# Optimization experiments

Hardware: AMD Instinct MI355X
Metric: run time of the kernel (lower is better)

The kernel has to match this reference:

```python
import jax, jax.numpy as jnp
import numpy as np

B, T, C = 2, 2048, 2048
H, HD = 16, 128  # num_heads, head_dim; inner_dim = H*HD = C
EPS = 1e-8


def _hadamard(n):
    # Sylvester construction, orthonormal scaling 1/sqrt(n)
    h = np.array([[1.0]], dtype=np.float32)
    while h.shape[0] < n:
        h = np.block([[h, h], [h, -h]])
    return jnp.asarray(h / np.sqrt(n), dtype=jnp.float32)


def _round_ste(x):
    # straight-through rounding (matches int8 training-time quantization semantics)
    return x + jax.lax.stop_gradient(jnp.round(x) - x)


def q8_linear(x, w):
    # dynamic per-token int8 activation quant + per-out-channel int8 weight quant
    s_x = jnp.max(jnp.abs(x), axis=-1, keepdims=True) / 127.0 + EPS   # (B,T,1)
    xq = _round_ste(jnp.clip(x / s_x, -127.0, 127.0))
    s_w = jnp.max(jnp.abs(w), axis=-1, keepdims=True) / 127.0 + EPS   # (O,1)
    wq = _round_ste(jnp.clip(w / s_w, -127.0, 127.0))
    return jnp.einsum('btk,ok->bto', xq, wq) * s_x * s_w[:, 0]


def rmsnorm(x, g, eps=1e-6):
    return x * jax.lax.rsqrt(jnp.mean(x * x, axis=-1, keepdims=True) + eps) * g


def apply_rope(x, cos, sin):
    # x: (B,T,H*HD); cos/sin: (T,HD/2); interleaved rotary per head
    b, t, c = x.shape
    xh = x.reshape(b, t, -1, HD)
    x1, x2 = xh[..., 0::2], xh[..., 1::2]
    co = cos[None, :, None, :]
    si = sin[None, :, None, :]
    o1 = x1 * co - x2 * si
    o2 = x1 * si + x2 * co
    out = jnp.stack([o1, o2], axis=-1).reshape(b, t, -1, HD)
    return out.reshape(b, t, c)


def setup_inputs() -> dict:
    key = jax.random.key(0)
    ks = jax.random.split(key, 8)
    hidden_states = jax.random.normal(ks[0], (B, T, C), jnp.float32)
    attention_mask = jax.random.randint(ks[1], (B,), 1, T + 1).astype(jnp.int32)  # valid lengths
    sc = 1.0 / np.sqrt(C)
    wq = jax.random.normal(ks[2], (H * HD, C), jnp.float32) * sc
    wk = jax.random.normal(ks[3], (H * HD, C), jnp.float32) * sc
    wv = jax.random.normal(ks[4], (H * HD, C), jnp.float32) * sc
    wo = jax.random.normal(ks[5], (C, H * HD), jnp.float32) * (1.0 / np.sqrt(H * HD))
    q_gamma = jnp.ones((H * HD,), jnp.float32)
    k_gamma = jnp.ones((H * HD,), jnp.float32)
    inv_freq = 1.0 / (10000.0 ** (np.arange(0, HD, 2, dtype=np.float32) / HD))
    freqs = np.outer(np.arange(T, dtype=np.float32), inv_freq)  # (T, HD/2)
    cos = jnp.asarray(np.cos(freqs), jnp.float32)
    sin = jnp.asarray(np.sin(freqs), jnp.float32)
    return {"hidden_states": hidden_states, "attention_mask": attention_mask,
            "wq": wq, "wk": wk, "wv": wv, "wo": wo,
            "q_gamma": q_gamma, "k_gamma": k_gamma, "cos": cos, "sin": sin}


def reference(hidden_states, attention_mask, wq, wk, wv, wo, q_gamma, k_gamma, cos, sin):
    b, t, c = hidden_states.shape
    q = rmsnorm(q8_linear(hidden_states, wq), q_gamma)
    k = rmsnorm(q8_linear(hidden_states, wk), k_gamma)
    v = q8_linear(hidden_states, wv)
    q = apply_rope(q, cos, sin)
    k = apply_rope(k, cos, sin)
    # (B,T,H*HD) -> (B,H,T,HD)
    q = q.reshape(b, t, H, HD).transpose(0, 2, 1, 3)
    k = k.reshape(b, t, H, HD).transpose(0, 2, 1, 3)
    v = v.reshape(b, t, H, HD).transpose(0, 2, 1, 3)
    # Hadamard rotation of q/k head dims (orthonormal -> preserves qk dot products)
    Hm = _hadamard(HD)
    qh = q @ Hm
    kh = k @ Hm
    scores = jnp.einsum('bhqd,bhkd->bhqk', qh, kh) * (1.0 / np.sqrt(HD))
    # ragged batch mask: keys beyond per-batch valid length are masked out
    valid = jnp.arange(t)[None, :] < attention_mask[:, None]   # (B,T)
    scores = jnp.where(valid[:, None, None, :], scores, -1e9)
    p = jax.nn.softmax(scores, axis=-1)
    o = jnp.einsum('bhqk,bhkd->bhqd', p, v)
    o = o.transpose(0, 2, 1, 3).reshape(b, t, c)
    return q8_linear(o, wo)
```

## Files before the change

kernel.cpp:

```cpp
#include <hip/hip_runtime.h>
#include <stdint.h>

typedef unsigned short u16;
typedef unsigned int u32;
typedef int v4i __attribute__((ext_vector_type(4)));
typedef float v4f __attribute__((ext_vector_type(4)));
typedef short v8s __attribute__((ext_vector_type(8)));

#define Bn 2
#define Tn 2048
#define Cn 2048
#define Hn 16
#define HDn 128

__device__ __forceinline__ float b2f(u16 u) {
    u32 x = ((u32)u) << 16;
    float f;
    __builtin_memcpy(&f, &x, 4);
    return f;
}
__device__ __forceinline__ u16 f2b(float f) {
    u32 x;
    __builtin_memcpy(&x, &f, 4);
    u32 r = (x + 0x7fffu + ((x >> 16) & 1u)) >> 16;
    return (u16)r;
}

__device__ __forceinline__ void async16(const void* g, void* l) {
    __builtin_amdgcn_global_load_lds(
        (const __attribute__((address_space(1))) u32*)g,
        (__attribute__((address_space(3))) u32*)l, 16, 0, 0);
}

__global__ __launch_bounds__(256) void quant_all(
    const float* __restrict__ w0, const float* __restrict__ w1,
    const float* __restrict__ w2, const float* __restrict__ w3,
    const float* __restrict__ hid, int8_t* __restrict__ Q,
    float* __restrict__ S) {
    int r = blockIdx.x;
    const float* src;
    int ro;
    if (r < 2048) { src = w0; ro = r; }
    else if (r < 4096) { src = w1; ro = r - 2048; }
    else if (r < 6144) { src = w2; ro = r - 4096; }
    else if (r < 8192) { src = w3; ro = r - 6144; }
    else { src = hid; ro = r - 8192; }
    const float* x = src + (size_t)ro * Cn;
    int tid = threadIdx.x;
    float4 v0 = ((const float4*)x)[tid * 2];
    float4 v1 = ((const float4*)x)[tid * 2 + 1];
    float a[8] = {v0.x, v0.y, v0.z, v0.w, v1.x, v1.y, v1.z, v1.w};
    float m = 0.f;
#pragma unroll
    for (int i = 0; i < 8; i++) m = fmaxf(m, fabsf(a[i]));
#pragma unroll
    for (int o = 32; o; o >>= 1) m = fmaxf(m, __shfl_xor(m, o));
    __shared__ float sm[4];
    if ((tid & 63) == 0) sm[tid >> 6] = m;
    __syncthreads();
    m = fmaxf(fmaxf(sm[0], sm[1]), fmaxf(sm[2], sm[3]));
    float s = m * (1.0f / 127.0f) + 1e-8f;
    if (tid == 0) S[r] = s;
    u32 lo = 0, hi = 0;
#pragma unroll
    for (int i = 0; i < 8; i++) {
        float q = rintf(fminf(127.f, fmaxf(-127.f, a[i] / s)));
        int qi = (int)q;
        u32 byte = (u32)(qi & 0xff);
        if (i < 4) lo |= byte << (8 * i);
        else hi |= byte << (8 * (i - 4));
    }
    u32* qp = (u32*)(Q + (size_t)r * Cn);
    qp[tid * 2] = lo;
    qp[tid * 2 + 1] = hi;
}

__global__ __launch_bounds__(256) void quant_rows(const float* __restrict__ X,
                                                  int8_t* __restrict__ Q,
                                                  float* __restrict__ S) {
    int r = blockIdx.x;
    const float* x = X + (size_t)r * Cn;
    int tid = threadIdx.x;
    float4 v0 = ((const float4*)x)[tid * 2];
    float4 v1 = ((const float4*)x)[tid * 2 + 1];
    float a[8] = {v0.x, v0.y, v0.z, v0.w, v1.x, v1.y, v1.z, v1.w};
    float m = 0.f;
#pragma unroll
    for (int i = 0; i < 8; i++) m = fmaxf(m, fabsf(a[i]));
#pragma unroll
    for (int o = 32; o; o >>= 1) m = fmaxf(m, __shfl_xor(m, o));
    __shared__ float sm[4];
    if ((tid & 63) == 0) sm[tid >> 6] = m;
    __syncthreads();
    m = fmaxf(fmaxf(sm[0], sm[1]), fmaxf(sm[2], sm[3]));
    float s = m * (1.0f / 127.0f) + 1e-8f;
    if (tid == 0) S[r] = s;
    u32 lo = 0, hi = 0;
#pragma unroll
    for (int i = 0; i < 8; i++) {
        float q = rintf(fminf(127.f, fmaxf(-127.f, a[i] / s)));
        int qi = (int)q;
        u32 byte = (u32)(qi & 0xff);
        if (i < 4) lo |= byte << (8 * i);
        else hi |= byte << (8 * (i - 4));
    }
    u32* qp = (u32*)(Q + (size_t)r * Cn);
    qp[tid * 2] = lo;
    qp[tid * 2 + 1] = hi;
}

__global__ __launch_bounds__(256) void gemm_i8(
    const int8_t* __restrict__ A, const int8_t* __restrict__ Bw,
    const float* __restrict__ sA, const float* __restrict__ sB,
    void* __restrict__ Co, long long bStride, long long sbStride,
    long long cStride, int fp32out) {
    int z = blockIdx.z;
    Bw += (size_t)z * bStride;
    sB += (size_t)z * sbStride;
    const int K = 2048, N = 2048;
    __shared__ int8_t As[128 * 64];
    __shared__ int8_t Bs[128 * 64];
    int m0 = blockIdx.x * 128, n0 = blockIdx.y * 128;
    int tid = threadIdx.x, w = tid >> 6, lane = tid & 63;
    int quad = lane >> 4, l15 = lane & 15;
    int wy = w >> 1, wx = w & 1;
    const v4i zi = {0, 0, 0, 0};
    v4i acc[4][4];
#pragma unroll
    for (int i = 0; i < 4; i++)
#pragma unroll
        for (int j = 0; j < 4; j++) acc[i][j] = zi;
    int lrow = lane >> 2;
    int slot = lane & 3;
    int srow = w * 32 + lrow;
    int klog = ((slot ^ (lrow & 3)) * 16);
    const int8_t* ga = A + (size_t)(m0 + srow) * K + klog;
    const int8_t* gb = Bw + (size_t)(n0 + srow) * K + klog;
    int8_t* la = &As[srow * 64 + slot * 16];
    int8_t* lb = &Bs[srow * 64 + slot * 16];
    for (int k0 = 0; k0 < K; k0 += 64) {
        async16(ga + k0, la);
        async16(ga + k0 + (size_t)16 * K, la + 16 * 64);
        async16(gb + k0, lb);
        async16(gb + k0 + (size_t)16 * K, lb + 16 * 64);
        __syncthreads();
        int swz = (quad ^ (l15 & 3)) * 16;
        v4i af[4], bf4[4];
#pragma unroll
        for (int i = 0; i < 4; i++)
            af[i] = *(const v4i*)&As[(wy * 64 + i * 16 + l15) * 64 + swz];
#pragma unroll
        for (int j = 0; j < 4; j++)
            bf4[j] = *(const v4i*)&Bs[(wx * 64 + j * 16 + l15) * 64 + swz];
#pragma unroll
        for (int i = 0; i < 4; i++)
#pragma unroll
            for (int j = 0; j < 4; j++)
                acc[i][j] = __builtin_amdgcn_mfma_i32_16x16x64_i8(
                    af[i], bf4[j], acc[i][j], 0, 0, 0);
        __syncthreads();
    }
#pragma unroll
    for (int i = 0; i < 4; i++) {
        int mb = m0 + wy * 64 + i * 16 + quad * 4;
        float s0 = sA[mb], s1 = sA[mb + 1], s2 = sA[mb + 2], s3 = sA[mb + 3];
#pragma unroll
        for (int j = 0; j < 4; j++) {
            int n = n0 + wx * 64 + j * 16 + l15;
            float sb = sB[n];
            if (fp32out) {
                float* cp = (float*)Co + (size_t)cStride * z + (size_t)mb * N + n;
                cp[0] = (float)acc[i][j][0] * s0 * sb;
                cp[N] = (float)acc[i][j][1] * s1 * sb;
                cp[2 * N] = (float)acc[i][j][2] * s2 * sb;
                cp[3 * N] = (float)acc[i][j][3] * s3 * sb;
            } else {
                u16* cp = (u16*)Co + (size_t)cStride * z + (size_t)mb * N + n;
                cp[0] = f2b((float)acc[i][j][0] * s0 * sb);
                cp[N] = f2b((float)acc[i][j][1] * s1 * sb);
                cp[2 * N] = f2b((float)acc[i][j][2] * s2 * sb);
                cp[3 * N] = f2b((float)acc[i][j][3] * s3 * sb);
            }
        }
    }
}

__global__ __launch_bounds__(256) void norm_rope2(u16* __restrict__ Qb,
                                                  u16* __restrict__ Kb,
                                                  const float* __restrict__ qg,
                                                  const float* __restrict__ kg,
                                                  const float* __restrict__ cs,
                                                  const float* __restrict__ sn) {
    int row = blockIdx.x;
    int isq = row < 4096;
    row &= 4095;
    u16* x = (isq ? Qb : Kb) + (size_t)row * Cn;
    const float* g = isq ? qg : kg;
    float ps = isq ? 0.08838834764831845f : 1.0f;
    int t = row & (Tn - 1);
    int tid = threadIdx.x;
    uint4 raw = ((const uint4*)x)[tid];
    u16 us[8];
    us[0] = raw.x & 0xffff; us[1] = raw.x >> 16;
    us[2] = raw.y & 0xffff; us[3] = raw.y >> 16;
    us[4] = raw.z & 0xffff; us[5] = raw.z >> 16;
    us[6] = raw.w & 0xffff; us[7] = raw.w >> 16;
    float v[8];
#pragma unroll
    for (int i = 0; i < 8; i++) v[i] = b2f(us[i]);
    float ss = 0.f;
#pragma unroll
    for (int i = 0; i < 8; i++) ss += v[i] * v[i];
#pragma unroll
    for (int o = 32; o; o >>= 1) ss += __shfl_xor(ss, o);
    __shared__ float sm[4];
    if ((tid & 63) == 0) sm[tid >> 6] = ss;
    __syncthreads();
    ss = sm[0] + sm[1] + sm[2] + sm[3];
    float r = rsqrtf(ss * (1.f / 2048.f) + 1e-6f) * ps;
    float4 g0 = ((const float4*)g)[tid * 2];
    float4 g1 = ((const float4*)g)[tid * 2 + 1];
    float n[8];
    n[0] = v[0] * r * g0.x; n[1] = v[1] * r * g0.y;
    n[2] = v[2] * r * g0.z; n[3] = v[3] * r * g0.w;
    n[4] = v[4] * r * g1.x; n[5] = v[5] * r * g1.y;
    n[6] = v[6] * r * g1.z; n[7] = v[7] * r * g1.w;
    int pi = (tid & 15) * 4;
    float4 c4 = *(const float4*)(cs + t * 64 + pi);
    float4 s4 = *(const float4*)(sn + t * 64 + pi);
    float o[8];
    o[0] = n[0] * c4.x - n[1] * s4.x; o[1] = n[0] * s4.x + n[1] * c4.x;
    o[2] = n[2] * c4.y - n[3] * s4.y; o[3] = n[2] * s4.y + n[3] * c4.y;
    o[4] = n[4] * c4.z - n[5] * s4.z; o[5] = n[4] * s4.z + n[5] * c4.z;
    o[6] = n[6] * c4.w - n[7] * s4.w; o[7] = n[6] * s4.w + n[7] * c4.w;
    uint4 out;
    out.x = (u32)f2b(o[0]) | ((u32)f2b(o[1]) << 16);
    out.y = (u32)f2b(o[2]) | ((u32)f2b(o[3]) << 16);
    out.z = (u32)f2b(o[4]) | ((u32)f2b(o[5]) << 16);
    out.w = (u32)f2b(o[6]) | ((u32)f2b(o[7]) << 16);
    ((uint4*)x)[tid] = out;
}

__global__ __launch_bounds__(256) void vtrans(const u16* __restrict__ V,
                                              u16* __restrict__ Vt) {
    int bh = blockIdx.y;
    int b = bh >> 4, h = bh & 15;
    int t0 = blockIdx.x * 64;
    __shared__ u32 tile[64][133];
    int tid = threadIdx.x;
    int r = tid >> 2, seg = (tid & 3) * 32;
    const uint4* src =
        (const uint4*)(V + ((size_t)b * Tn + t0 + r) * Cn + h * HDn + seg);
#pragma unroll
    for (int i = 0; i < 4; i++) {
        uint4 u = src[i];
        u32 uu[4] = {u.x, u.y, u.z, u.w};
#pragma unroll
        for (int j = 0; j < 4; j++) {
            tile[r][seg + i * 8 + j * 2] = uu[j] & 0xffff;
            tile[r][seg + i * 8 + j * 2 + 1] = uu[j] >> 16;
        }
    }
    __syncthreads();
    int d = tid >> 1, tseg = (tid & 1) * 32;
    u16* dst = Vt + ((size_t)bh * HDn + d) * Tn + t0 + tseg;
#pragma unroll
    for (int i = 0; i < 4; i++) {
        u32 p0 = tile[tseg + i * 8 + 0][d] | (tile[tseg + i * 8 + 1][d] << 16);
        u32 p1 = tile[tseg + i * 8 + 2][d] | (tile[tseg + i * 8 + 3][d] << 16);
        u32 p2 = tile[tseg + i * 8 + 4][d] | (tile[tseg + i * 8 + 5][d] << 16);
        u32 p3 = tile[tseg + i * 8 + 6][d] | (tile[tseg + i * 8 + 7][d] << 16);
        ((uint4*)dst)[i] = make_uint4(p0, p1, p2, p3);
    }
}

__global__ __launch_bounds__(256, 3) void flash(const u16* __restrict__ Qb,
                                                const u16* __restrict__ Kb,
                                                const u16* __restrict__ Vt,
                                                const int* __restrict__ mask,
                                                float* __restrict__ O) {
    int qt = blockIdx.x, bh = blockIdx.y;
    int b = bh >> 4, h = bh & 15;
    int L = mask[b];
    int nkfull = L >> 6;
    int nk = (L + 63) >> 6;
    __shared__ u16 Ks[2][64 * 128];
    __shared__ u16 Ps[2][64 * 72];
    __shared__ float sred[256];
    __shared__ float sinv[64];
    int tid = threadIdx.x, w = tid >> 6, lane = tid & 63;
    int quad = lane >> 4, l15 = lane & 15;

    v8s aq[4][4];
#pragma unroll
    for (int i = 0; i < 4; i++)
#pragma unroll
        for (int kk = 0; kk < 4; kk++)
            aq[i][kk] = *(const v8s*)(Qb +
                                      ((size_t)b * Tn + qt * 64 + i * 16 + l15) * Cn +
                                      h * HDn + kk * 32 + quad * 8);

    const u16* ksp[4];
    int kdo[4];
#pragma unroll
    for (int cc = 0; cc < 4; cc++) {
        int c = w * 4 + cc;
        int rk = c * 4 + (lane >> 4);
        int sk = lane & 15;
        int lgk = sk ^ (rk & 7);
        ksp[cc] = Kb + ((size_t)b * Tn + rk) * Cn + h * HDn + lgk * 8;
        kdo[cc] = rk * 128 + sk * 8;
    }

    const u16* vp0 = Vt + ((size_t)bh * HDn + 2 * w * 16 + l15) * Tn + quad * 8;
    const u16* vp1 = vp0 + 16 * Tn;

    float sum16[16];
#pragma unroll
    for (int j = 0; j < 16; j++) sum16[j] = 0.f;
    const v4f zf = {0.f, 0.f, 0.f, 0.f};
    v4f oacc[4][2];
#pragma unroll
    for (int m = 0; m < 4; m++) {
        oacc[m][0] = zf;
        oacc[m][1] = zf;
    }

#pragma unroll
    for (int cc = 0; cc < 4; cc++) {
        async16(ksp[cc], &Ks[0][kdo[cc]]);
        ksp[cc] += (size_t)64 * Cn;
    }
    __syncthreads();

    int cur = 0;
    for (int kt = 0; kt < nk; kt++) {
        if (kt + 1 < nk) {
#pragma unroll
            for (int cc = 0; cc < 4; cc++) {
                async16(ksp[cc], &Ks[cur ^ 1][kdo[cc]]);
                ksp[cc] += (size_t)64 * Cn;
            }
        }
        v8s bv00 = *(const v8s*)(vp0);
        v8s bv10 = *(const v8s*)(vp0 + 32);
        v8s bv01 = *(const v8s*)(vp1);
        v8s bv11 = *(const v8s*)(vp1 + 32);
        vp0 += 64;
        vp1 += 64;
        v4f sacc[4] = {zf, zf, zf, zf};
        const u16* krow = &Ks[cur][(w * 16 + l15) * 128];
#pragma unroll
        for (int kk = 0; kk < 4; kk++) {
            v8s bk = *(const v8s*)(krow + ((((kk * 4 + quad) ^ (l15 & 7))) << 3));
#pragma unroll
            for (int i = 0; i < 4; i++)
                sacc[i] = __builtin_amdgcn_mfma_f32_16x16x32_bf16(aq[i][kk], bk,
                                                                  sacc[i], 0, 0, 0);
        }
        bool valid = (kt < nkfull) || ((kt * 64 + w * 16 + l15) < L);
#pragma unroll
        for (int i = 0; i < 4; i++)
#pragma unroll
            for (int r2 = 0; r2 < 4; r2++) {
                float p = valid ? __expf(sacc[i][r2]) : 0.f;
                sum16[i * 4 + r2] += p;
                Ps[cur][(i * 16 + quad * 4 + r2) * 72 + w * 16 + l15] = f2b(p);
            }
        __syncthreads();
#pragma unroll
        for (int kk2 = 0; kk2 < 2; kk2++) {
            v8s ap[4];
#pragma unroll
            for (int m = 0; m < 4; m++)
                ap[m] = *(const v8s*)(&Ps[cur][(m * 16 + l15) * 72 + kk2 * 32 +
                                               quad * 8]);
            v8s bva = kk2 ? bv10 : bv00;
            v8s bvb = kk2 ? bv11 : bv01;
#pragma unroll
            for (int m = 0; m < 4; m++) {
                oacc[m][0] = __builtin_amdgcn_mfma_f32_16x16x32_bf16(
                    ap[m], bva, oacc[m][0], 0, 0, 0);
                oacc[m][1] = __builtin_amdgcn_mfma_f32_16x16x32_bf16(
                    ap[m], bvb, oacc[m][1], 0, 0, 0);
            }
        }
        cur ^= 1;
    }
#pragma unroll
    for (int j = 0; j < 16; j++) {
        float s = sum16[j];
        s += __shfl_xor(s, 1);
        s += __shfl_xor(s, 2);
        s += __shfl_xor(s, 4);
        s += __shfl_xor(s, 8);
        sum16[j] = s;
    }
    if (l15 == 0) {
#pragma unroll
        for (int i = 0; i < 4; i++)
#pragma unroll
            for (int r2 = 0; r2 < 4; r2++)
                sred[w * 64 + i * 16 + quad * 4 + r2] = sum16[i * 4 + r2];
    }
    __syncthreads();
    if (tid < 64)
        sinv[tid] =
            1.f / (sred[tid] + sred[64 + tid] + sred[128 + tid] + sred[192 + tid]);
    __syncthreads();
#pragma unroll
    for (int m = 0; m < 4; m++)
#pragma unroll
        for (int r2 = 0; r2 < 4; r2++) {
            float inv = sinv[m * 16 + quad * 4 + r2];
            int row = qt * 64 + m * 16 + quad * 4 + r2;
#pragma unroll
            for (int nbi = 0; nbi < 2; nbi++) {
                int d = h * HDn + (2 * w + nbi) * 16 + l15;
                O[((size_t)b * Tn + row) * Cn + d] = oacc[m][nbi][r2] * inv;
            }
        }
}

extern "C" void kernel_launch(void* const* d_in, const int* in_sizes, int n_in,
                              void* d_out, int out_size, void* d_ws,
                              size_t ws_size, hipStream_t stream) {
    const float* hidden = (const float*)d_in[0];
    const int* mask = (const int*)d_in[1];
    const float* wq = (const float*)d_in[2];
    const float* wk = (const float*)d_in[3];
    const float* wv = (const float*)d_in[4];
    const float* wo = (const float*)d_in[5];
    const float* qg = (const float*)d_in[6];
    const float* kg = (const float*)d_in[7];
    const float* cs = (const float*)d_in[8];
    const float* sn = (const float*)d_in[9];

    char* ws = (char*)d_ws;
    int8_t* q8 = (int8_t*)(ws);
    float* sAll = (float*)(ws + 25165824);
    u16* qb = (u16*)(ws + 25214976);
    u16* kb = (u16*)(ws + 41992192);
    u16* vb = (u16*)(ws + 58769408);
    u16* vt = (u16*)(ws + 75546624);
    float* Obuf = (float*)(ws + 92323840);
    int8_t* hid8 = q8 + 16777216;
    float* sx = sAll + 8192;

    quant_all<<<12288, 256, 0, stream>>>(wq, wk, wv, wo, hidden, q8, sAll);

    gemm_i8<<<dim3(32, 16, 3), 256, 0, stream>>>(hid8, q8, sx, sAll, (void*)qb,
                                                 4194304LL, 2048LL, 8388608LL, 0);

    norm_rope2<<<8192, 256, 0, stream>>>(qb, kb, qg, kg, cs, sn);
    vtrans<<<dim3(32, 32), 256, 0, stream>>>(vb, vt);

    flash<<<dim3(32, 32), 256, 0, stream>>>(qb, kb, vt, mask, Obuf);

    quant_rows<<<4096, 256, 0, stream>>>(Obuf, hid8, sx);
    gemm_i8<<<dim3(32, 16, 1), 256, 0, stream>>>(hid8, q8 + 12582912, sx,
                                                 sAll + 6144, d_out, 0LL, 0LL,
                                                 0LL, 1);
}
```

Measured before the change: 340.1 us.

## Software-pipeline flash attention PV with next QK tile, remap block ids

Restructures the flash attention loop so that the P·V MFMAs for the previous key tile run in the same phase as the QK^T MFMAs for the current tile. This removes one __syncthreads per tile and lets the exp/softmax work overlap with matrix work, with s_setprio raised around the MFMA section. The loop is unrolled by two to use fixed Ps and Ks buffer indices, and a final epilogue handles the last tile's P·V. Block indices are also remapped to a 1D grid that groups eight heads per query tile, which should improve L2 reuse of K/V. The cost is more register pressure and more complex code.

Measured after the change: 371.6 us. 9.2% more time.

```diff
diff --git a/kernel.cpp b/kernel.cpp
--- a/kernel.cpp
+++ b/kernel.cpp
@@ -274,12 +274,68 @@
     }
 }
 
+#define FLASH_TILE(KT, CUR)                                                     \
+    do {                                                                        \
+        int kt_ = (KT);                                                         \
+        if (kt_ + 1 < nk) {                                                     \
+            _Pragma("unroll") for (int cc = 0; cc < 4; cc++) {                  \
+                async16(ksp[cc], &Ks[(CUR) ^ 1][kdo[cc]]);                      \
+                ksp[cc] += (size_t)64 * Cn;                                     \
+            }                                                                   \
+        }                                                                       \
+        v8s bp0, bp1, bp2, bp3;                                                 \
+        if (kt_) {                                                              \
+            bp0 = *(const v8s*)(vp0);                                           \
+            bp1 = *(const v8s*)(vp0 + 32);                                      \
+            bp2 = *(const v8s*)(vp1);                                           \
+            bp3 = *(const v8s*)(vp1 + 32);                                      \
+            vp0 += 64;                                                          \
+            vp1 += 64;                                                          \
+        }                                                                       \
+        v4f sacc[4] = {zf, zf, zf, zf};                                         \
+        const u16* krow = &Ks[CUR][(w * 16 + l15) * 128];                       \
+        __builtin_amdgcn_s_setprio(1);                                          \
+        _Pragma("unroll") for (int kk = 0; kk < 4; kk++) {                      \
+            v8s bk = *(const v8s*)(krow + ((((kk * 4 + quad) ^ (l15 & 7))) << 3)); \
+            _Pragma("unroll") for (int i = 0; i < 4; i++)                       \
+                sacc[i] = __builtin_amdgcn_mfma_f32_16x16x32_bf16(              \
+                    aq[i][kk], bk, sacc[i], 0, 0, 0);                           \
+        }                                                                       \
+        if (kt_) {                                                              \
+            _Pragma("unroll") for (int kk2 = 0; kk2 < 2; kk2++) {               \
+                v8s ap[4];                                                      \
+                _Pragma("unroll") for (int m = 0; m < 4; m++)                   \
+                    ap[m] = *(const v8s*)(&Ps[(CUR) ^ 1][(m * 16 + l15) * 72 +  \
+                                                         kk2 * 32 + quad * 8]); \
+                v8s bva = kk2 ? bp1 : bp0;                                      \
+                v8s bvb = kk2 ? bp3 : bp2;                                      \
+                _Pragma("unroll") for (int m = 0; m < 4; m++) {                 \
+                    oacc[m][0] = __builtin_amdgcn_mfma_f32_16x16x32_bf16(       \
+                        ap[m], bva, oacc[m][0], 0, 0, 0);                       \
+                    oacc[m][1] = __builtin_amdgcn_mfma_f32_16x16x32_bf16(       \
+                        ap[m], bvb, oacc[m][1], 0, 0, 0);                       \
+                }                                                               \
+            }                                                                   \
+        }                                                                       \
+        __builtin_amdgcn_s_setprio(0);                                          \
+        bool valid = (kt_ < nkfull) || ((kt_ * 64 + w * 16 + l15) < L);         \
+        _Pragma("unroll") for (int i = 0; i < 4; i++)                           \
+            _Pragma("unroll") for (int r2 = 0; r2 < 4; r2++) {                  \
+                float p = valid ? __expf(sacc[i][r2]) : 0.f;                    \
+                sum16[i * 4 + r2] += p;                                         \
+                Ps[CUR][(i * 16 + quad * 4 + r2) * 72 + w * 16 + l15] = f2b(p); \
+            }                                                                   \
+        __syncthreads();                                                        \
+    } while (0)
+
 __global__ __launch_bounds__(256, 3) void flash(const u16* __restrict__ Qb,
                                                 const u16* __restrict__ Kb,
                                                 const u16* __restrict__ Vt,
                                                 const int* __restrict__ mask,
                                                 float* __restrict__ O) {
-    int qt = blockIdx.x, bh = blockIdx.y;
+    int id = blockIdx.x;
+    int bh = (id & 7) + 8 * (id >> 8);
+    int qt = (id >> 3) & 31;
     int b = bh >> 4, h = bh & 15;
     int L = mask[b];
     int nkfull = L >> 6;
@@ -333,50 +389,26 @@
     }
     __syncthreads();
 
-    int cur = 0;
-    for (int kt = 0; kt < nk; kt++) {
-        if (kt + 1 < nk) {
-#pragma unroll
-            for (int cc = 0; cc < 4; cc++) {
-                async16(ksp[cc], &Ks[cur ^ 1][kdo[cc]]);
-                ksp[cc] += (size_t)64 * Cn;
-            }
-        }
-        v8s bv00 = *(const v8s*)(vp0);
-        v8s bv10 = *(const v8s*)(vp0 + 32);
-        v8s bv01 = *(const v8s*)(vp1);
-        v8s bv11 = *(const v8s*)(vp1 + 32);
-        vp0 += 64;
-        vp1 += 64;
-        v4f sacc[4] = {zf, zf, zf, zf};
-        const u16* krow = &Ks[cur][(w * 16 + l15) * 128];
-#pragma unroll
-        for (int kk = 0; kk < 4; kk++) {
-            v8s bk = *(const v8s*)(krow + ((((kk * 4 + quad) ^ (l15 & 7))) << 3));
-#pragma unroll
-            for (int i = 0; i < 4; i++)
-                sacc[i] = __builtin_amdgcn_mfma_f32_16x16x32_bf16(aq[i][kk], bk,
-                                                                  sacc[i], 0, 0, 0);
-        }
-        bool valid = (kt < nkfull) || ((kt * 64 + w * 16 + l15) < L);
-#pragma unroll
-        for (int i = 0; i < 4; i++)
-#pragma unroll
-            for (int r2 = 0; r2 < 4; r2++) {
-                float p = valid ? __expf(sacc[i][r2]) : 0.f;
-                sum16[i * 4 + r2] += p;
-                Ps[cur][(i * 16 + quad * 4 + r2) * 72 + w * 16 + l15] = f2b(p);
-            }
-        __syncthreads();
+    for (int kt2 = 0; kt2 < nk; kt2 += 2) {
+        FLASH_TILE(kt2, 0);
+        if (kt2 + 1 < nk) FLASH_TILE(kt2 + 1, 1);
+    }
+
+    {
+        v8s bp0 = *(const v8s*)(vp0);
+        v8s bp1 = *(const v8s*)(vp0 + 32);
+        v8s bp2 = *(const v8s*)(vp1);
+        v8s bp3 = *(const v8s*)(vp1 + 32);
+        const u16* pfin = &Ps[(nk - 1) & 1][0];
 #pragma unroll
         for (int kk2 = 0; kk2 < 2; kk2++) {
             v8s ap[4];
 #pragma unroll
             for (int m = 0; m < 4; m++)
-                ap[m] = *(const v8s*)(&Ps[cur][(m * 16 + l15) * 72 + kk2 * 32 +
-                                               quad * 8]);
-            v8s bva = kk2 ? bv10 : bv00;
-            v8s bvb = kk2 ? bv11 : bv01;
+                ap[m] = *(const v8s*)(pfin + (m * 16 + l15) * 72 + kk2 * 32 +
+                                      quad * 8);
+            v8s bva = kk2 ? bp1 : bp0;
+            v8s bvb = kk2 ? bp3 : bp2;
 #pragma unroll
             for (int m = 0; m < 4; m++) {
                 oacc[m][0] = __builtin_amdgcn_mfma_f32_16x16x32_bf16(
@@ -385,7 +417,6 @@
                     ap[m], bvb, oacc[m][1], 0, 0, 0);
             }
         }
-        cur ^= 1;
     }
 #pragma unroll
     for (int j = 0; j < 16; j++) {
@@ -455,7 +486,7 @@
     norm_rope2<<<8192, 256, 0, stream>>>(qb, kb, qg, kg, cs, sn);
     vtrans<<<dim3(32, 32), 256, 0, stream>>>(vb, vt);
 
-    flash<<<dim3(32, 32), 256, 0, stream>>>(qb, kb, vt, mask, Obuf);
+    flash<<<dim3(1024), 256, 0, stream>>>(qb, kb, vt, mask, Obuf);
 
     quant_rows<<<4096, 256, 0, stream>>>(Obuf, hid8, sx);
     gemm_i8<<<dim3(32, 16, 1), 256, 0, stream>>>(hid8, q8 + 12582912, sx,
```
